# Kernel tuning notes

Measured on AMD Instinct MI355X. Metric: run time of the kernel, lower is better.

The kernel has to match this reference:

```python
import jax, jax.numpy as jnp
import numpy as np

H = 1024
N_HEADS = 16
DK = H // N_HEADS
B = 4
S_TGT = 1024
S_SRC = 1024
LN_EPS = 1e-5


def _ln(x, g, b):
    m = jnp.mean(x, axis=-1, keepdims=True)
    v = jnp.mean(jnp.square(x - m), axis=-1, keepdims=True)
    return (x - m) * jax.lax.rsqrt(v + LN_EPS) * g + b


def _mha(q_in, k_in, v_in, wq, wk, wv, wo, mask):
    # Equivalent to torch split(hidden//n_splits)+cat(dim=0) head layout:
    # per-(batch,head) scaled dot-product attention.
    Bq, Sq, _ = q_in.shape
    Sk = k_in.shape[1]
    q = (q_in @ wq).reshape(Bq, Sq, N_HEADS, DK)
    k = (k_in @ wk).reshape(Bq, Sk, N_HEADS, DK)
    v = (v_in @ wv).reshape(Bq, Sk, N_HEADS, DK)
    scores = jnp.einsum('bqhd,bkhd->bhqk', q, k)
    if mask is not None:
        scores = jnp.where(mask[:, None, :, :], -jnp.inf, scores)
    attn = jax.nn.softmax(scores / np.sqrt(DK).astype(np.float32), axis=-1)
    ctx = jnp.einsum('bhqk,bkhd->bqhd', attn, v).reshape(Bq, Sq, H)
    return ctx @ wo


def setup_inputs() -> dict:
    key = jax.random.key(0)
    ks = jax.random.split(key, 16)
    std = 1.0 / np.sqrt(H)
    p = {
        'x': jax.random.normal(ks[0], (B, S_TGT, H), jnp.float32),
        'key_and_value': jax.random.normal(ks[1], (B, S_SRC, H), jnp.float32),
        'mask': jnp.zeros((B, S_TGT, S_SRC), jnp.bool_),  # no padding
        # causal mask: True above the diagonal (masked positions)
        'future_mask': jnp.broadcast_to(
            jnp.triu(jnp.ones((S_TGT, S_TGT), jnp.bool_), k=1), (B, S_TGT, S_TGT)),
        'sa_wq': jax.random.normal(ks[2], (H, H), jnp.float32) * std,
        'sa_wk': jax.random.normal(ks[3], (H, H), jnp.float32) * std,
        'sa_wv': jax.random.normal(ks[4], (H, H), jnp.float32) * std,
        'sa_wo': jax.random.normal(ks[5], (H, H), jnp.float32) * std,
        'ca_wq': jax.random.normal(ks[6], (H, H), jnp.float32) * std,
        'ca_wk': jax.random.normal(ks[7], (H, H), jnp.float32) * std,
        'ca_wv': jax.random.normal(ks[8], (H, H), jnp.float32) * std,
        'ca_wo': jax.random.normal(ks[9], (H, H), jnp.float32) * std,
        'fc_w1': jax.random.normal(ks[10], (H, 4 * H), jnp.float32) * std,
        'fc_b1': jnp.zeros((4 * H,), jnp.float32),
        'fc_w2': jax.random.normal(ks[11], (4 * H, H), jnp.float32) * (0.5 * std),
        'fc_b2': jnp.zeros((H,), jnp.float32),
        'ln1_g': jnp.ones((H,), jnp.float32), 'ln1_b': jnp.zeros((H,), jnp.float32),
        'ln2_g': jnp.ones((H,), jnp.float32), 'ln2_b': jnp.zeros((H,), jnp.float32),
        'ln3_g': jnp.ones((H,), jnp.float32), 'ln3_b': jnp.zeros((H,), jnp.float32),
    }
    return p


def reference(x, key_and_value, mask, future_mask,
              sa_wq, sa_wk, sa_wv, sa_wo,
              ca_wq, ca_wk, ca_wv, ca_wo,
              fc_w1, fc_b1, fc_w2, fc_b2,
              ln1_g, ln1_b, ln2_g, ln2_b, ln3_g, ln3_b):
    # prev is None path (training); dropout in eval mode = identity.
    z = _ln(x, ln1_g, ln1_b)
    z = x + _mha(z, z, z, sa_wq, sa_wk, sa_wv, sa_wo, future_mask)
    nkv = _ln(key_and_value, ln2_g, ln2_b)
    z = z + _mha(_ln(z, ln2_g, ln2_b), nkv, nkv, ca_wq, ca_wk, ca_wv, ca_wo, mask)
    h = jax.nn.relu(_ln(z, ln3_g, ln3_b) @ fc_w1 + fc_b1)
    z = z + (h @ fc_w2 + fc_b2)
    return z
```

## Files before the change

### kernel.cpp

```cpp
#include <hip/hip_runtime.h>
#include <hip/hip_bf16.h>

typedef __attribute__((ext_vector_type(8))) short short8;
typedef __attribute__((ext_vector_type(4))) float f32x4;
using bf16 = __hip_bfloat16;

__device__ __forceinline__ void gload16(const void* g, void* l) {
  __builtin_amdgcn_global_load_lds(
      (const __attribute__((address_space(1))) void*)g,
      (__attribute__((address_space(3))) void*)l, 16, 0, 0);
}

__device__ __forceinline__ short f2bf(float f) {
  bf16 h = __float2bfloat16(f);
  short s;
  __builtin_memcpy(&s, &h, 2);
  return s;
}

__global__ __launch_bounds__(256)
void wtr8(const float* w0, const float* w1, const float* w2, const float* w3,
          const float* w4, const float* w5, const float* w6, const float* w7,
          bf16* __restrict__ Wout) {
  __shared__ float tile[32][33];
  const float* w;
  switch (blockIdx.z) {
    case 0: w = w0; break; case 1: w = w1; break;
    case 2: w = w2; break; case 3: w = w3; break;
    case 4: w = w4; break; case 5: w = w5; break;
    case 6: w = w6; break; default: w = w7; break;
  }
  bf16* wt = Wout + (size_t)blockIdx.z * 1024 * 1024;
  const int tx = threadIdx.x & 31, ty = threadIdx.x >> 5;
  const int c0 = blockIdx.x * 32, r0 = blockIdx.y * 32;
#pragma unroll
  for (int i = 0; i < 4; ++i)
    tile[ty * 4 + i][tx] = w[(size_t)(r0 + ty * 4 + i) * 1024 + c0 + tx];
  __syncthreads();
#pragma unroll
  for (int i = 0; i < 4; ++i) {
    const int cc = ty * 4 + i;
    wt[(size_t)(c0 + cc) * 1024 + r0 + tx] = __float2bfloat16(tile[tx][cc]);
  }
}

__global__ __launch_bounds__(256)
void wtr(const float* __restrict__ w, bf16* __restrict__ wt, int R, int C) {
  __shared__ float tile[32][33];
  const int tx = threadIdx.x & 31, ty = threadIdx.x >> 5;
  const int c0 = blockIdx.x * 32, r0 = blockIdx.y * 32;
#pragma unroll
  for (int i = 0; i < 4; ++i)
    tile[ty * 4 + i][tx] = w[(size_t)(r0 + ty * 4 + i) * C + c0 + tx];
  __syncthreads();
#pragma unroll
  for (int i = 0; i < 4; ++i) {
    const int cc = ty * 4 + i;
    wt[(size_t)(c0 + cc) * R + r0 + tx] = __float2bfloat16(tile[tx][cc]);
  }
}

__global__ __launch_bounds__(256)
void ln_k(const float* __restrict__ x, const float* __restrict__ g,
          const float* __restrict__ b, bf16* __restrict__ y) {
  const int row = blockIdx.x, t = threadIdx.x;
  const int wv = t >> 6, l = t & 63;
  const float4 v = reinterpret_cast<const float4*>(x + (size_t)row * 1024)[t];
  float s = v.x + v.y + v.z + v.w;
  float s2 = v.x * v.x + v.y * v.y + v.z * v.z + v.w * v.w;
#pragma unroll
  for (int m = 1; m < 64; m <<= 1) {
    s += __shfl_xor(s, m, 64);
    s2 += __shfl_xor(s2, m, 64);
  }
  __shared__ float ps[4], ps2[4];
  if (l == 0) { ps[wv] = s; ps2[wv] = s2; }
  __syncthreads();
  s = ps[0] + ps[1] + ps[2] + ps[3];
  s2 = ps2[0] + ps2[1] + ps2[2] + ps2[3];
  const float mean = s * (1.f / 1024.f);
  const float var = s2 * (1.f / 1024.f) - mean * mean;
  const float rs = rsqrtf(var + 1e-5f);
  const float4 gg = reinterpret_cast<const float4*>(g)[t];
  const float4 bb = reinterpret_cast<const float4*>(b)[t];
  ushort4 o;
  o.x = (unsigned short)f2bf((v.x - mean) * rs * gg.x + bb.x);
  o.y = (unsigned short)f2bf((v.y - mean) * rs * gg.y + bb.y);
  o.z = (unsigned short)f2bf((v.z - mean) * rs * gg.z + bb.z);
  o.w = (unsigned short)f2bf((v.w - mean) * rs * gg.w + bb.w);
  reinterpret_cast<ushort4*>(y + (size_t)row * 1024)[t] = o;
}

template <int BM, int EPI>
__global__ __launch_bounds__(256, 2)
void gemm_bt(const bf16* __restrict__ A, const bf16* __restrict__ BT,
             const float* bias, const float* res, void* outp,
             int M, int N, int K, bf16* vtp, int nv0) {
  constexpr int WM = BM / 32;
  constexpr int APASS = BM / 32;
  __shared__ alignas(16) short al[2][BM * 64];
  __shared__ alignas(16) short bl[2][128 * 64];
  const int t = threadIdx.x;
  const int gx = N >> 7;
  const int nwg = gridDim.x * gridDim.y;
  int id = blockIdx.y * gridDim.x + blockIdx.x;
  id = (id & 7) * (nwg >> 3) + (id >> 3);
  const int bx = id % gx, by = id / gx;
  const int m0 = by * BM, n0 = bx * 128;
  const int wv = t >> 6, l = t & 63, lr = l & 15, lk = l >> 4;
  const int wr = wv >> 1, wc = wv & 1;
  const int tr = t >> 3, tc = (t & 7) * 8;
  const int tcs = (((t & 7) ^ (tr & 7)) * 8);
  const int cro0 = ((lk ^ (lr & 7)) * 8);
  const int cro1 = (((4 + lk) ^ (lr & 7)) * 8);

  f32x4 acc[WM][4];
#pragma unroll
  for (int i = 0; i < WM; ++i)
#pragma unroll
    for (int j = 0; j < 4; ++j) acc[i][j] = (f32x4)0.f;

#define STAGE(buf, k0)                                                        \
  do {                                                                        \
    _Pragma("unroll") for (int it = 0; it < APASS; ++it) {                    \
      const int row = it * 32 + tr;                                           \
      gload16(A + (size_t)(m0 + row) * K + (k0) + tcs,                        \
              (char*)&al[buf][row * 64 + tc]);                                \
    }                                                                         \
    _Pragma("unroll") for (int it = 0; it < 4; ++it) {                        \
      const int row = it * 32 + tr;                                           \
      gload16(BT + (size_t)(n0 + row) * K + (k0) + tcs,                       \
              (char*)&bl[buf][row * 64 + tc]);                                \
    }                                                                         \
  } while (0)

#define COMPUTE(cur)                                                          \
  do {                                                                        \
    _Pragma("unroll") for (int ks = 0; ks < 2; ++ks) {                        \
      const int cro = ks ? cro1 : cro0;                                       \
      short8 af[WM], bfv[4];                                                  \
      _Pragma("unroll") for (int m = 0; m < WM; ++m) af[m] =                  \
          *reinterpret_cast<const short8*>(                                   \
              &al[cur][(wr * (BM / 2) + m * 16 + lr) * 64 + cro]);            \
      _Pragma("unroll") for (int n = 0; n < 4; ++n) bfv[n] =                  \
          *reinterpret_cast<const short8*>(                                   \
              &bl[cur][(wc * 64 + n * 16 + lr) * 64 + cro]);                  \
      _Pragma("unroll") for (int m = 0; m < WM; ++m)                          \
          _Pragma("unroll") for (int n = 0; n < 4; ++n) acc[m][n] =           \
              __builtin_amdgcn_mfma_f32_16x16x32_bf16(af[m], bfv[n],          \
                                                      acc[m][n], 0, 0, 0);    \
    }                                                                         \
  } while (0)

  const int nt = K >> 6;
  if constexpr (BM == 64) {
    STAGE(0, 0);
    STAGE(1, 64);
    for (int tk = 0; tk < nt; ++tk) {
      const int cur = tk & 1;
      if (tk < nt - 1)
        asm volatile("s_waitcnt vmcnt(6)" ::: "memory");
      else
        asm volatile("s_waitcnt vmcnt(0)" ::: "memory");
      __builtin_amdgcn_s_barrier();
      COMPUTE(cur);
      if (tk + 2 < nt) {
        asm volatile("s_waitcnt lgkmcnt(0)" ::: "memory");
        __builtin_amdgcn_s_barrier();
        STAGE(cur, (tk + 2) << 6);
      }
    }
  } else {
    STAGE(0, 0);
    asm volatile("s_waitcnt vmcnt(0)" ::: "memory");
    __syncthreads();
    for (int tk = 0; tk < nt; ++tk) {
      const int cur = tk & 1;
      if (tk + 1 < nt) STAGE(cur ^ 1, (tk + 1) << 6);
      COMPUTE(cur);
      asm volatile("s_waitcnt vmcnt(0)" ::: "memory");
      __syncthreads();
    }
  }
#undef STAGE
#undef COMPUTE

  const int r0 = m0 + wr * (BM / 2), c0 = n0 + wc * 64;
  if constexpr (EPI == 4) {
#pragma unroll
    for (int m = 0; m < WM; ++m) {
      const int rowb = r0 + m * 16 + lk * 4;
      const int bb = rowb >> 10, s0 = rowb & 1023;
#pragma unroll
      for (int n = 0; n < 4; ++n) {
        const int col = c0 + n * 16 + lr;
        if (col < nv0) {
#pragma unroll
          for (int r = 0; r < 4; ++r)
            ((bf16*)outp)[(size_t)(rowb + r) * nv0 + col] =
                __float2bfloat16(acc[m][n][r]);
        } else {
          ushort4 u;
          u.x = (unsigned short)f2bf(acc[m][n][0]);
          u.y = (unsigned short)f2bf(acc[m][n][1]);
          u.z = (unsigned short)f2bf(acc[m][n][2]);
          u.w = (unsigned short)f2bf(acc[m][n][3]);
          const size_t vidx = ((size_t)bb * 1024 + (col - nv0)) * 1024 + s0;
          *reinterpret_cast<ushort4*>(vtp + vidx) = u;
        }
      }
    }
  } else {
#pragma unroll
    for (int m = 0; m < WM; ++m)
#pragma unroll
      for (int n = 0; n < 4; ++n) {
        const int col = c0 + n * 16 + lr;
#pragma unroll
        for (int r = 0; r < 4; ++r) {
          const int row = r0 + m * 16 + lk * 4 + r;
          const size_t idx = (size_t)row * N + col;
          float v = acc[m][n][r];
          if (EPI == 0) {
            ((bf16*)outp)[idx] = __float2bfloat16(v);
          } else if (EPI == 1) {
            ((float*)outp)[idx] = res[idx] + v;
          } else if (EPI == 2) {
            v += bias[col];
            ((bf16*)outp)[idx] = __float2bfloat16(fmaxf(v, 0.f));
          } else {
            ((float*)outp)[idx] = res[idx] + v + bias[col];
          }
        }
      }
  }
}

__global__ __launch_bounds__(512, 1)
void gemm256(const bf16* __restrict__ A, const bf16* __restrict__ BT,
             const float* __restrict__ bias, bf16* __restrict__ outp,
             int M, int N, int K) {
  __shared__ alignas(16) short al[2][256 * 64];
  __shared__ alignas(16) short bl[2][256 * 64];
  const int t = threadIdx.x;
  const int gx = N >> 8;
  const int nwg = gridDim.x * gridDim.y;
  int id = blockIdx.y * gridDim.x + blockIdx.x;
  id = (id & 7) * (nwg >> 3) + (id >> 3);
  const int bx = id % gx, by = id / gx;
  const int m0 = by * 256, n0 = bx * 256;
  const int wid = t >> 6, l = t & 63, lr = l & 15, lk = l >> 4;
  const int wm = wid >> 2, wn = wid & 3;
  const int tr = t >> 3, tc = (t & 7) * 8;
  const int tcs = (((t & 7) ^ (tr & 7)) * 8);
  const int cro0 = ((lk ^ (lr & 7)) * 8);
  const int cro1 = (((4 + lk) ^ (lr & 7)) * 8);

  f32x4 acc[8][4];
#pragma unroll
  for (int i = 0; i < 8; ++i)
#pragma unroll
    for (int j = 0; j < 4; ++j) acc[i][j] = (f32x4)0.f;

#define STAGE2(buf, k0)                                                       \
  do {                                                                        \
    _Pragma("unroll") for (int it = 0; it < 4; ++it) {                        \
      const int row = it * 64 + tr;                                           \
      gload16(A + (size_t)(m0 + row) * K + (k0) + tcs,                        \
              (char*)&al[buf][row * 64 + tc]);                                \
    }                                                                         \
    _Pragma("unroll") for (int it = 0; it < 4; ++it) {                        \
      const int row = it * 64 + tr;                                           \
      gload16(BT + (size_t)(n0 + row) * K + (k0) + tcs,                       \
              (char*)&bl[buf][row * 64 + tc]);                                \
    }                                                                         \
  } while (0)

#define COMPUTE2(cur)                                                         \
  do {                                                                        \
    _Pragma("unroll") for (int ks = 0; ks < 2; ++ks) {                        \
      const int cro = ks ? cro1 : cro0;                                       \
      short8 af[8], bfv[4];                                                   \
      _Pragma("unroll") for (int m = 0; m < 8; ++m) af[m] =                   \
          *reinterpret_cast<const short8*>(                                   \
              &al[cur][(wm * 128 + m * 16 + lr) * 64 + cro]);                 \
      _Pragma("unroll") for (int n = 0; n < 4; ++n) bfv[n] =                  \
          *reinterpret_cast<const short8*>(                                   \
              &bl[cur][(wn * 64 + n * 16 + lr) * 64 + cro]);                  \
      _Pragma("unroll") for (int m = 0; m < 8; ++m)                           \
          _Pragma("unroll") for (int n = 0; n < 4; ++n) acc[m][n] =           \
              __builtin_amdgcn_mfma_f32_16x16x32_bf16(af[m], bfv[n],          \
                                                      acc[m][n], 0, 0, 0);    \
    }                                                                         \
  } while (0)

  const int nt = K >> 6;
  STAGE2(0, 0);
  STAGE2(1, 64);
  for (int tk = 0; tk < nt; ++tk) {
    const int cur = tk & 1;
    if (tk < nt - 1)
      asm volatile("s_waitcnt vmcnt(8)" ::: "memory");
    else
      asm volatile("s_waitcnt vmcnt(0)" ::: "memory");
    __builtin_amdgcn_s_barrier();
    COMPUTE2(cur);
    if (tk + 2 < nt) {
      asm volatile("s_waitcnt lgkmcnt(0)" ::: "memory");
      __builtin_amdgcn_s_barrier();
      STAGE2(cur, (tk + 2) << 6);
    }
  }
#undef STAGE2
#undef COMPUTE2

  const int r0 = m0 + wm * 128, c0 = n0 + wn * 64;
#pragma unroll
  for (int m = 0; m < 8; ++m)
#pragma unroll
    for (int n = 0; n < 4; ++n) {
      const int col = c0 + n * 16 + lr;
      const float bcol = bias[col];
#pragma unroll
      for (int r = 0; r < 4; ++r) {
        const int row = r0 + m * 16 + lk * 4 + r;
        const float v = acc[m][n][r] + bcol;
        outp[(size_t)row * N + col] = __float2bfloat16(fmaxf(v, 0.f));
      }
    }
}

template <bool CAUSAL>
__global__ __launch_bounds__(256, 2)
void flash8(const bf16* __restrict__ Qb, int ldq,
            const bf16* __restrict__ Kb, int ldk,
            const bf16* __restrict__ VTb, bf16* __restrict__ Ob) {
  __shared__ alignas(16) short kl[3][64 * 64];
  __shared__ alignas(16) short vl[3][64 * 64];
  __shared__ alignas(16) short pl[4][32 * 72];
  const int t = threadIdx.x, wv = t >> 6, l = t & 63, lr = l & 15, lk = l >> 4;
  const int raw = blockIdx.y * 8 + blockIdx.x;
  const int id = (raw & 7) * 64 + (raw >> 3);
  const int qb = id & 7, bh = id >> 3;
  const int b = bh >> 4, h = bh & 15;
  const size_t rowbase = (size_t)b * 1024;
  const int q0 = qb * 128 + wv * 32;
  const bf16* Vbase = VTb + (rowbase + h * 64) * 1024;

  const int tr = t >> 3;
  const int tcd = (t & 7) * 8;
  const int tcs = (((t & 7) ^ (tr & 7)) * 8);
  const int cro0 = ((lk ^ (lr & 7)) * 8);
  const int cro1 = (((4 + lk) ^ (lr & 7)) * 8);

  short8 qf[2][2];
#pragma unroll
  for (int m = 0; m < 2; ++m)
#pragma unroll
    for (int ks = 0; ks < 2; ++ks)
      qf[m][ks] = *reinterpret_cast<const short8*>(
          Qb + (rowbase + q0 + m * 16 + lr) * ldq + h * 64 + ks * 32 + lk * 8);

  short8 ones;
#pragma unroll
  for (int j = 0; j < 8; ++j) ones[j] = (short)0x3F80;

  f32x4 accO[2][4];
  f32x4 accL[2];
#pragma unroll
  for (int m = 0; m < 2; ++m) {
#pragma unroll
    for (int n = 0; n < 4; ++n) accO[m][n] = (f32x4)0.f;
    accL[m] = (f32x4)0.f;
  }

  const int ntb = CAUSAL ? (qb * 2 + 2) : 16;
  const int myLast = q0 >> 6;

#define FSTAGE(buf, kv0)                                                      \
  do {                                                                        \
    _Pragma("unroll") for (int it = 0; it < 2; ++it) {                        \
      const int row = it * 32 + tr;                                           \
      gload16(Kb + (rowbase + (kv0) + row) * ldk + h * 64 + tcs,              \
              (char*)&kl[buf][row * 64 + tcd]);                               \
    }                                                                         \
    _Pragma("unroll") for (int it = 0; it < 2; ++it) {                        \
      const int row = it * 32 + tr;                                           \
      gload16(Vbase + (size_t)row * 1024 + (kv0) + tcs,                       \
              (char*)&vl[buf][row * 64 + tcd]);                               \
    }                                                                         \
  } while (0)

  FSTAGE(0, 0);
  FSTAGE(1, 64);
  int cur = 0;
  for (int tk = 0; tk < ntb; ++tk) {
    if (tk < ntb - 1)
      asm volatile("s_waitcnt vmcnt(4)" ::: "memory");
    else
      asm volatile("s_waitcnt vmcnt(0)" ::: "memory");
    __builtin_amdgcn_s_barrier();
    if (tk + 2 < ntb) {
      int stg = cur + 2;
      if (stg >= 3) stg -= 3;
      FSTAGE(stg, (tk + 2) << 6);
    }
    if (!CAUSAL || tk <= myLast) {
      const int kv0 = tk * 64;
      const bool needmask = CAUSAL && (tk == myLast);
      f32x4 sa[2][4];
#pragma unroll
      for (int m = 0; m < 2; ++m)
#pragma unroll
        for (int n = 0; n < 4; ++n) sa[m][n] = (f32x4)0.f;
#pragma unroll
      for (int ks = 0; ks < 2; ++ks) {
        const int cro = ks ? cro1 : cro0;
        short8 kf[4];
#pragma unroll
        for (int n = 0; n < 4; ++n)
          kf[n] = *reinterpret_cast<const short8*>(
              &kl[cur][(n * 16 + lr) * 64 + cro]);
        __builtin_amdgcn_s_setprio(1);
#pragma unroll
        for (int m = 0; m < 2; ++m)
#pragma unroll
          for (int n = 0; n < 4; ++n)
            sa[m][n] = __builtin_amdgcn_mfma_f32_16x16x32_bf16(
                qf[m][ks], kf[n], sa[m][n], 0, 0, 0);
        __builtin_amdgcn_s_setprio(0);
      }
#pragma unroll
      for (int m = 0; m < 2; ++m) {
#pragma unroll
        for (int r = 0; r < 4; ++r) {
          const int row = q0 + m * 16 + lk * 4 + r;
          float s0 = sa[m][0][r] * 0.125f, s1 = sa[m][1][r] * 0.125f;
          float s2 = sa[m][2][r] * 0.125f, s3 = sa[m][3][r] * 0.125f;
          if (needmask) {
            if (kv0 + 0 + lr > row) s0 = -1e30f;
            if (kv0 + 16 + lr > row) s1 = -1e30f;
            if (kv0 + 32 + lr > row) s2 = -1e30f;
            if (kv0 + 48 + lr > row) s3 = -1e30f;
          }
          const float p0 = __expf(s0), p1 = __expf(s1);
          const float p2 = __expf(s2), p3 = __expf(s3);
          const int prow = m * 16 + lk * 4 + r;
          pl[wv][prow * 72 + lr + 0] = f2bf(p0);
          pl[wv][prow * 72 + lr + 16] = f2bf(p1);
          pl[wv][prow * 72 + lr + 32] = f2bf(p2);
          pl[wv][prow * 72 + lr + 48] = f2bf(p3);
        }
      }
#pragma unroll
      for (int ks = 0; ks < 2; ++ks) {
        const int cro = ks ? cro1 : cro0;
        short8 pf[2], vf[4];
#pragma unroll
        for (int m = 0; m < 2; ++m)
          pf[m] = *reinterpret_cast<const short8*>(
              &pl[wv][(m * 16 + lr) * 72 + ks * 32 + lk * 8]);
#pragma unroll
        for (int n = 0; n < 4; ++n)
          vf[n] = *reinterpret_cast<const short8*>(
              &vl[cur][(n * 16 + lr) * 64 + cro]);
        __builtin_amdgcn_s_setprio(1);
#pragma unroll
        for (int m = 0; m < 2; ++m) {
#pragma unroll
          for (int n = 0; n < 4; ++n)
            accO[m][n] = __builtin_amdgcn_mfma_f32_16x16x32_bf16(
                pf[m], vf[n], accO[m][n], 0, 0, 0);
          accL[m] = __builtin_amdgcn_mfma_f32_16x16x32_bf16(
              pf[m], ones, accL[m], 0, 0, 0);
        }
        __builtin_amdgcn_s_setprio(0);
      }
    }
    cur = (cur + 1 == 3) ? 0 : cur + 1;
  }
#undef FSTAGE

#pragma unroll
  for (int m = 0; m < 2; ++m)
#pragma unroll
    for (int n = 0; n < 4; ++n)
#pragma unroll
      for (int r = 0; r < 4; ++r) {
        const int row = q0 + m * 16 + lk * 4 + r;
        const int col = n * 16 + lr;
        const float o = accO[m][n][r] / accL[m][r];
        Ob[(rowbase + row) * 1024 + h * 64 + col] = __float2bfloat16(o);
      }
}

extern "C" void kernel_launch(void* const* d_in, const int* in_sizes, int n_in,
                              void* d_out, int out_size, void* d_ws,
                              size_t ws_size, hipStream_t stream) {
  const float* x = (const float*)d_in[0];
  const float* kv_in = (const float*)d_in[1];
  const float* sa_wq = (const float*)d_in[4];
  const float* sa_wk = (const float*)d_in[5];
  const float* sa_wv = (const float*)d_in[6];
  const float* sa_wo = (const float*)d_in[7];
  const float* ca_wq = (const float*)d_in[8];
  const float* ca_wk = (const float*)d_in[9];
  const float* ca_wv = (const float*)d_in[10];
  const float* ca_wo = (const float*)d_in[11];
  const float* fc_w1 = (const float*)d_in[12];
  const float* fc_b1 = (const float*)d_in[13];
  const float* fc_w2 = (const float*)d_in[14];
  const float* fc_b2 = (const float*)d_in[15];
  const float* ln1_g = (const float*)d_in[16];
  const float* ln1_b = (const float*)d_in[17];
  const float* ln2_g = (const float*)d_in[18];
  const float* ln2_b = (const float*)d_in[19];
  const float* ln3_g = (const float*)d_in[20];
  const float* ln3_b = (const float*)d_in[21];

  char* ws = (char*)d_ws;
  const size_t MB = 1024 * 1024;
  bf16* W = (bf16*)ws;
  bf16* w1T = W + 8 * MB;
  bf16* w2T = W + 12 * MB;
  float* z = (float*)(ws + 32 * MB);
  bf16* t0 = (bf16*)(ws + 48 * MB);
  bf16* qkvb = (bf16*)(ws + 56 * MB);
  bf16* vts = (bf16*)(ws + 72 * MB);
  bf16* kb = (bf16*)(ws + 80 * MB);
  bf16* vtc = (bf16*)(ws + 88 * MB);
  bf16* qb = (bf16*)(ws + 96 * MB);
  bf16* ctx = (bf16*)(ws + 104 * MB);
  bf16* kvln = (bf16*)(ws + 112 * MB);
  bf16* hb = (bf16*)(ws + 120 * MB);

  const dim3 B256(256);
  wtr8<<<dim3(32, 32, 8), B256, 0, stream>>>(sa_wq, sa_wk, sa_wv, sa_wo,
                                             ca_wq, ca_wk, ca_wv, ca_wo, W);
  wtr<<<dim3(128, 32), B256, 0, stream>>>(fc_w1, w1T, 1024, 4096);
  wtr<<<dim3(32, 128), B256, 0, stream>>>(fc_w2, w2T, 4096, 1024);

  ln_k<<<4096, B256, 0, stream>>>(x, ln1_g, ln1_b, t0);
  gemm_bt<128, 4><<<dim3(24, 32), B256, 0, stream>>>(
      t0, W, nullptr, nullptr, qkvb, 4096, 3072, 1024, vts, 2048);
  flash8<true><<<dim3(8, 64), B256, 0, stream>>>(
      qkvb, 2048, qkvb + 1024, 2048, vts, ctx);
  gemm_bt<64, 1><<<dim3(8, 64), B256, 0, stream>>>(
      ctx, W + 3 * MB, nullptr, x, z, 4096, 1024, 1024, nullptr, 0);

  ln_k<<<4096, B256, 0, stream>>>(kv_in, ln2_g, ln2_b, kvln);
  ln_k<<<4096, B256, 0, stream>>>(z, ln2_g, ln2_b, t0);
  gemm_bt<128, 4><<<dim3(16, 32), B256, 0, stream>>>(
      kvln, W + 5 * MB, nullptr, nullptr, kb, 4096, 2048, 1024, vtc, 1024);
  gemm_bt<64, 0><<<dim3(8, 64), B256, 0, stream>>>(
      t0, W + 4 * MB, nullptr, nullptr, qb, 4096, 1024, 1024, nullptr, 0);
  flash8<false><<<dim3(8, 64), B256, 0, stream>>>(
      qb, 1024, kb, 1024, vtc, ctx);
  gemm_bt<64, 1><<<dim3(8, 64), B256, 0, stream>>>(
      ctx, W + 7 * MB, nullptr, z, z, 4096, 1024, 1024, nullptr, 0);

  ln_k<<<4096, B256, 0, stream>>>(z, ln3_g, ln3_b, t0);
  gemm256<<<dim3(16, 16), dim3(512), 0, stream>>>(
      t0, w1T, fc_b1, hb, 4096, 4096, 1024);
  gemm_bt<64, 3><<<dim3(8, 64), B256, 0, stream>>>(
      hb, w2T, fc_b2, z, d_out, 4096, 1024, 4096, nullptr, 0);
}
```

Baseline: 335.5 us.

## Split-K the FC2 GEMM over the large-tile kernel and add a reduction pass

The second FFN GEMM (K=4096) now runs on the 256x256-tile gemm256 kernel, split into four K-chunks along grid z. Each chunk writes its fp32 partial result to the workspace. A new elementwise kernel then sums the four partials with the residual and the bias. The aim is to use the more efficient large-tile kernel with a full single-wave grid, at the cost of roughly 64MB of extra partial-sum writes and reads plus one more launch.

Result: no change. 337.1 us (+0.5%).

```diff
diff --git a/kernel.cpp b/kernel.cpp
--- a/kernel.cpp
+++ b/kernel.cpp
@@ -89,6 +89,22 @@
   o.z = (unsigned short)f2bf((v.z - mean) * rs * gg.z + bb.z);
   o.w = (unsigned short)f2bf((v.w - mean) * rs * gg.w + bb.w);
   reinterpret_cast<ushort4*>(y + (size_t)row * 1024)[t] = o;
+}
+
+__global__ __launch_bounds__(256)
+void ffn_add4(const float4* __restrict__ p0, const float4* __restrict__ p1,
+              const float4* __restrict__ p2, const float4* __restrict__ p3,
+              const float4* __restrict__ res, const float4* __restrict__ bias,
+              float4* __restrict__ out) {
+  const size_t i = (size_t)blockIdx.x * 256 + threadIdx.x;
+  const float4 a = p0[i], b = p1[i], c = p2[i], d = p3[i], r = res[i];
+  const float4 g = bias[i & 255];
+  float4 o;
+  o.x = (a.x + b.x) + (c.x + d.x) + r.x + g.x;
+  o.y = (a.y + b.y) + (c.y + d.y) + r.y + g.y;
+  o.z = (a.z + b.z) + (c.z + d.z) + r.z + g.z;
+  o.w = (a.w + b.w) + (c.w + d.w) + r.w + g.w;
+  out[i] = o;
 }
 
 template <int BM, int EPI>
@@ -236,10 +252,11 @@
   }
 }
 
+template <int EPI>
 __global__ __launch_bounds__(512, 1)
 void gemm256(const bf16* __restrict__ A, const bf16* __restrict__ BT,
-             const float* __restrict__ bias, bf16* __restrict__ outp,
-             int M, int N, int K) {
+             const float* __restrict__ bias, void* __restrict__ outp,
+             int M, int N, int K, int lda) {
   __shared__ alignas(16) short al[2][256 * 64];
   __shared__ alignas(16) short bl[2][256 * 64];
   const int t = threadIdx.x;
@@ -256,6 +273,9 @@
   const int cro0 = ((lk ^ (lr & 7)) * 8);
   const int cro1 = (((4 + lk) ^ (lr & 7)) * 8);
 
+  const bf16* Ab = (EPI == 5) ? A + (size_t)blockIdx.z * K : A;
+  const bf16* BTb = (EPI == 5) ? BT + (size_t)blockIdx.z * K : BT;
+
   f32x4 acc[8][4];
 #pragma unroll
   for (int i = 0; i < 8; ++i)
@@ -266,12 +286,12 @@
   do {                                                                        \
     _Pragma("unroll") for (int it = 0; it < 4; ++it) {                        \
       const int row = it * 64 + tr;                                           \
-      gload16(A + (size_t)(m0 + row) * K + (k0) + tcs,                        \
+      gload16(Ab + (size_t)(m0 + row) * lda + (k0) + tcs,                     \
               (char*)&al[buf][row * 64 + tc]);                                \
     }                                                                         \
     _Pragma("unroll") for (int it = 0; it < 4; ++it) {                        \
       const int row = it * 64 + tr;                                           \
-      gload16(BT + (size_t)(n0 + row) * K + (k0) + tcs,                       \
+      gload16(BTb + (size_t)(n0 + row) * lda + (k0) + tcs,                    \
               (char*)&bl[buf][row * 64 + tc]);                                \
     }                                                                         \
   } while (0)
@@ -315,19 +335,35 @@
 #undef COMPUTE2
 
   const int r0 = m0 + wm * 128, c0 = n0 + wn * 64;
-#pragma unroll
-  for (int m = 0; m < 8; ++m)
-#pragma unroll
-    for (int n = 0; n < 4; ++n) {
-      const int col = c0 + n * 16 + lr;
-      const float bcol = bias[col];
-#pragma unroll
-      for (int r = 0; r < 4; ++r) {
-        const int row = r0 + m * 16 + lk * 4 + r;
-        const float v = acc[m][n][r] + bcol;
-        outp[(size_t)row * N + col] = __float2bfloat16(fmaxf(v, 0.f));
-      }
-    }
+  if constexpr (EPI == 2) {
+#pragma unroll
+    for (int m = 0; m < 8; ++m)
+#pragma unroll
+      for (int n = 0; n < 4; ++n) {
+        const int col = c0 + n * 16 + lr;
+        const float bcol = bias[col];
+#pragma unroll
+        for (int r = 0; r < 4; ++r) {
+          const int row = r0 + m * 16 + lk * 4 + r;
+          const float v = acc[m][n][r] + bcol;
+          ((bf16*)outp)[(size_t)row * N + col] =
+              __float2bfloat16(fmaxf(v, 0.f));
+        }
+      }
+  } else {
+    float* po = (float*)outp + (size_t)blockIdx.z * M * N;
+#pragma unroll
+    for (int m = 0; m < 8; ++m)
+#pragma unroll
+      for (int n = 0; n < 4; ++n) {
+        const int col = c0 + n * 16 + lr;
+#pragma unroll
+        for (int r = 0; r < 4; ++r) {
+          const int row = r0 + m * 16 + lk * 4 + r;
+          po[(size_t)row * N + col] = acc[m][n][r];
+        }
+      }
+  }
 }
 
 template <bool CAUSAL>
@@ -533,6 +569,7 @@
   bf16* ctx = (bf16*)(ws + 104 * MB);
   bf16* kvln = (bf16*)(ws + 112 * MB);
   bf16* hb = (bf16*)(ws + 120 * MB);
+  float* parts = (float*)(ws + 56 * MB);
 
   const dim3 B256(256);
   wtr8<<<dim3(32, 32, 8), B256, 0, stream>>>(sa_wq, sa_wk, sa_wv, sa_wo,
@@ -560,8 +597,14 @@
       ctx, W + 7 * MB, nullptr, z, z, 4096, 1024, 1024, nullptr, 0);
 
   ln_k<<<4096, B256, 0, stream>>>(z, ln3_g, ln3_b, t0);
-  gemm256<<<dim3(16, 16), dim3(512), 0, stream>>>(
-      t0, w1T, fc_b1, hb, 4096, 4096, 1024);
-  gemm_bt<64, 3><<<dim3(8, 64), B256, 0, stream>>>(
-      hb, w2T, fc_b2, z, d_out, 4096, 1024, 4096, nullptr, 0);
-}
+  gemm256<2><<<dim3(16, 16), dim3(512), 0, stream>>>(
+      t0, w1T, fc_b1, hb, 4096, 4096, 1024, 1024);
+  gemm256<5><<<dim3(4, 16, 4), dim3(512), 0, stream>>>(
+      hb, w2T, nullptr, parts, 4096, 1024, 1024, 4096);
+  ffn_add4<<<4096, B256, 0, stream>>>(
+      (const float4*)(parts + 0 * 4096 * 1024),
+      (const float4*)(parts + 1 * (size_t)4096 * 1024),
+      (const float4*)(parts + 2 * (size_t)4096 * 1024),
+      (const float4*)(parts + 3 * (size_t)4096 * 1024),
+      (const float4*)z, (const float4*)fc_b2, (float4*)d_out);
+}
```
